# Kernel optimization log

Hardware: AMD Instinct MI355X
Metric: run time of the kernel (lower is better)

## Reference

```python
import jax, jax.numpy as jnp
import numpy as np

K = 1024
H = 128

def setup_inputs() -> dict:
    key = jax.random.key(0)
    ks = jax.random.split(key, 11)
    s = lambda fan_in: 1.0 / np.sqrt(fan_in)
    # coord_mlp: Linear(H, H//2) -> GELU -> Linear(H//2, 2)
    cW1 = jax.random.uniform(ks[0], (H, H // 2), minval=-s(H), maxval=s(H))
    cb1 = jax.random.uniform(ks[1], (H // 2,), minval=-s(H), maxval=s(H))
    cW2 = jax.random.uniform(ks[2], (H // 2, 2), minval=-s(H // 2), maxval=s(H // 2))
    cb2 = jax.random.uniform(ks[3], (2,), minval=-s(H // 2), maxval=s(H // 2))
    # edge_mlp: Linear(2H, H) -> GELU -> Linear(H, H//2) -> GELU -> Linear(H//2, 1)
    eW1 = jax.random.uniform(ks[4], (2 * H, H), minval=-s(2 * H), maxval=s(2 * H))
    eb1 = jax.random.uniform(ks[5], (H,), minval=-s(2 * H), maxval=s(2 * H))
    eW2 = jax.random.uniform(ks[6], (H, H // 2), minval=-s(H), maxval=s(H))
    eb2 = jax.random.uniform(ks[7], (H // 2,), minval=-s(H), maxval=s(H))
    eW3 = jax.random.uniform(ks[8], (H // 2, 1), minval=-s(H // 2), maxval=s(H // 2))
    eb3 = jax.random.uniform(ks[9], (1,), minval=-s(H // 2), maxval=s(H // 2))
    z_s = jax.random.normal(ks[10], (K, H), dtype=jnp.float32)
    return {"z_s": z_s, "cW1": cW1, "cb1": cb1, "cW2": cW2, "cb2": cb2,
            "eW1": eW1, "eb1": eb1, "eW2": eW2, "eb2": eb2, "eW3": eW3, "eb3": eb3}

def reference(z_s, cW1, cb1, cW2, cb2, eW1, eb1, eW2, eb2, eW3, eb3):
    gelu = lambda x: jax.nn.gelu(x, approximate=False)  # torch default GELU is exact erf form
    # coords: [k, 2]
    coords_pred = gelu(z_s @ cW1 + cb1) @ cW2 + cb2
    # edge first layer: cat([zi, zj]) @ eW1 == zi @ eW1[:H] + zj @ eW1[H:]
    # (same math as the broadcast-concat, without materializing [k, k, 2H])
    pi = z_s @ eW1[:H]   # [k, H]
    pj = z_s @ eW1[H:]   # [k, H]
    h1 = gelu(pi[:, None, :] + pj[None, :, :] + eb1)   # [k, k, H]
    h2 = gelu(h1 @ eW2 + eb2)                          # [k, k, H//2]
    adj_logits = (h2 @ eW3 + eb3)[..., 0]              # [k, k]
    adj_logits = (adj_logits + adj_logits.T) / 2.0
    return (coords_pred, adj_logits)
```

## Files before the change

### kernel.cpp

```cpp
#include <hip/hip_runtime.h>
#include <hip/hip_fp16.h>


#define KN 1024
#define HN 128

typedef float  floatx4 __attribute__((ext_vector_type(4)));
typedef _Float16 half8v __attribute__((ext_vector_type(8)));
typedef _Float16 half2v __attribute__((ext_vector_type(2)));

__device__ __forceinline__ float gelu_f(float x) {
    float x2 = x * x;
    float t  = fmaf(x2, -0.1029434f, -2.3022087f);
    float e  = __builtin_amdgcn_exp2f(x * t);
    return x * __builtin_amdgcn_rcpf(e + 1.0f);
}

__device__ __forceinline__ unsigned int gelu2u(unsigned int xu) {
    __half2 x  = __builtin_bit_cast(__half2, xu);
    __half2 x2 = __hmul2(x, x);
    __half2 t  = __hfma2(x2, __float2half2_rn(-0.1029434f),
                             __float2half2_rn(-2.3022087f));
    __half2 e  = h2exp2(__hmul2(x, t));
    __half2 r  = h2rcp(__hadd2(e, __float2half2_rn(1.0f)));
    return __builtin_bit_cast(unsigned int, __hmul2(x, r));
}

__device__ __forceinline__ unsigned int cvt2u(float a, float b) {
    return __builtin_bit_cast(unsigned int, __builtin_amdgcn_cvt_pkrtz(a, b));
}

__global__ __launch_bounds__(256) void prep_kernel(
    const float* __restrict__ z,   const float* __restrict__ cW1,
    const float* __restrict__ cb1, const float* __restrict__ cW2,
    const float* __restrict__ cb2, const float* __restrict__ eW1,
    const float* __restrict__ eb1, const float* __restrict__ eW2,
    const float* __restrict__ eW3,
    _Float16* __restrict__ pi_h,   _Float16* __restrict__ pj_h,
    _Float16* __restrict__ w2T,    _Float16* __restrict__ w3h,
    float* __restrict__ coords ) {
    __shared__ float z8[8][128];
    __shared__ float c1s[8][64];
    const int tid = threadIdx.x;
    const int r0  = blockIdx.x * 8;

    if (blockIdx.x < 32) {
        int e = blockIdx.x * 256 + tid;
        int d = e >> 7, k = e & 127;
        int R = ((d >> 5) & 1) * 32 + ((d >> 2) & 1) * 16 +
                ((d >> 3) & 3) * 4  + (d & 3);
        w2T[R * 128 + k] = (_Float16)eW2[k * 64 + d];
    }
    if (blockIdx.x == 32 && tid < 64) w3h[tid] = (_Float16)eW3[tid];

#pragma unroll
    for (int s = 0; s < 4; ++s) {
        int e = tid + 256 * s;
        z8[e >> 7][e & 127] = z[r0 * HN + e];
    }
    __syncthreads();

    const int col = tid & 127, which = tid >> 7;
    const float* w = eW1 + which * HN * HN + col;
    float acc8[8] = {0.f, 0.f, 0.f, 0.f, 0.f, 0.f, 0.f, 0.f};
    for (int k = 0; k < HN; ++k) {
        float wv = w[k * HN];
#pragma unroll
        for (int r = 0; r < 8; ++r) acc8[r] = fmaf(z8[r][k], wv, acc8[r]);
    }
    if (which == 0) {
        float b = eb1[col];
#pragma unroll
        for (int r = 0; r < 8; ++r)
            pi_h[(r0 + r) * HN + col] = (_Float16)(acc8[r] + b);
    } else {
#pragma unroll
        for (int r = 0; r < 8; ++r)
            pj_h[(r0 + r) * HN + col] = (_Float16)acc8[r];
    }

#pragma unroll
    for (int s = 0; s < 2; ++s) {
        int task = tid + 256 * s;
        int row = task >> 6, mid = task & 63;
        float a = cb1[mid];
        for (int k = 0; k < HN; ++k) a = fmaf(z8[row][k], cW1[k * 64 + mid], a);
        c1s[row][mid] = gelu_f(a);
    }
    __syncthreads();
    if (tid < 16) {
        int row = tid >> 1, o = tid & 1;
        float a = cb2[o];
#pragma unroll 8
        for (int m = 0; m < 64; ++m) a = fmaf(c1s[row][m], cW2[m * 2 + o], a);
        coords[(r0 + row) * 2 + o] = a;
    }
}

__global__ __launch_bounds__(512, 7) void edge_kernel(
    const _Float16* __restrict__ pi_h, const _Float16* __restrict__ pj_h,
    const _Float16* __restrict__ w2T,  const _Float16* __restrict__ w3h,
    const float* __restrict__ eb2,     const float* __restrict__ eb3,
    float* __restrict__ out_adj) {
    __shared__ __align__(16) unsigned int pi_s[32 * 64];
    __shared__ __align__(16) unsigned int pj_s[16 * 64];
    __shared__ __align__(16) unsigned int w2_s[64 * 64];
    const int i0 = blockIdx.y * 32, j0 = blockIdx.x * 16;
    const int tid = threadIdx.x;

    const unsigned int* piu = (const unsigned int*)pi_h;
    const unsigned int* pju = (const unsigned int*)pj_h;
    const unsigned int* w2u = (const unsigned int*)w2T;

#pragma unroll
    for (int s = 0; s < 4; ++s) {
        int e = tid + 512 * s;
        int r = e >> 6;
        pi_s[e ^ ((r & 7) << 2)] = piu[(i0 + r) * 64 + (e & 63)];
    }
#pragma unroll
    for (int s = 0; s < 2; ++s) {
        int e = tid + 512 * s;
        int r = e >> 6;
        pj_s[e ^ ((r & 7) << 2)] = pju[(j0 + r) * 64 + (e & 63)];
    }
#pragma unroll
    for (int s = 0; s < 8; ++s) {
        int e = tid + 512 * s;
        int r = e >> 6;
        w2_s[e ^ ((r & 7) << 2)] = w2u[e];
    }

    const int lane = tid & 63;
    const int wave = tid >> 6;
    const int lrow = lane & 15;
    const int lhi  = lane >> 4;
    const int lhi4 = lhi << 2;
    const int lhi8 = lhi << 3;
    const int swzJ = (lrow & 7) << 2;

    const unsigned int* pjrow  = &pj_s[lrow << 6];
    const unsigned int* w2base = &w2_s[lrow << 6];

    const half8v w3f0 = *reinterpret_cast<const half8v*>(&w3h[lhi8]);
    const half8v w3f1 = *reinterpret_cast<const half8v*>(&w3h[32 + lhi8]);
    const float4 e0 = *reinterpret_cast<const float4*>(&eb2[lhi8]);
    const float4 e1 = *reinterpret_cast<const float4*>(&eb2[lhi8 + 4]);
    const float4 e2 = *reinterpret_cast<const float4*>(&eb2[32 + lhi8]);
    const float4 e3 = *reinterpret_cast<const float4*>(&eb2[36 + lhi8]);
    const float b3 = eb3[0];
    __syncthreads();

#pragma unroll
    for (int t = 0; t < 4; ++t) {
        const int iL = (wave << 2) + t;
        const unsigned int* pirow = &pi_s[iL << 6];
        const int swzI = (iL & 7) << 2;

        floatx4 acc[4];
        acc[0] = (floatx4){e0.x, e0.y, e0.z, e0.w};
        acc[1] = (floatx4){e1.x, e1.y, e1.z, e1.w};
        acc[2] = (floatx4){e2.x, e2.y, e2.z, e2.w};
        acc[3] = (floatx4){e3.x, e3.y, e3.z, e3.w};

#pragma unroll
        for (int q = 0; q < 4; ++q) {
            const int ko = (q << 4) + lhi4;
            half8v a = *reinterpret_cast<const half8v*>(&pirow[ko ^ swzI]);
            half8v b = *reinterpret_cast<const half8v*>(&pjrow[ko ^ swzJ]);
            uint4 su = __builtin_bit_cast(uint4, a + b);
            uint4 gu;
            gu.x = gelu2u(su.x);
            gu.y = gelu2u(su.y);
            gu.z = gelu2u(su.z);
            gu.w = gelu2u(su.w);
            half8v af = __builtin_bit_cast(half8v, gu);
            const int kw = ko ^ swzJ;
#pragma unroll
            for (int c = 0; c < 4; ++c) {
                half8v bf = *reinterpret_cast<const half8v*>(
                    &w2base[(c << 10) + kw]);
                acc[c] = __builtin_amdgcn_mfma_f32_16x16x32_f16(
                    bf, af, acc[c], 0, 0, 0);
            }
        }

        uint4 u0, u1;
        u0.x = gelu2u(cvt2u(acc[0][0], acc[0][1]));
        u0.y = gelu2u(cvt2u(acc[0][2], acc[0][3]));
        u0.z = gelu2u(cvt2u(acc[1][0], acc[1][1]));
        u0.w = gelu2u(cvt2u(acc[1][2], acc[1][3]));
        u1.x = gelu2u(cvt2u(acc[2][0], acc[2][1]));
        u1.y = gelu2u(cvt2u(acc[2][2], acc[2][3]));
        u1.z = gelu2u(cvt2u(acc[3][0], acc[3][1]));
        u1.w = gelu2u(cvt2u(acc[3][2], acc[3][3]));
        half8v h20 = __builtin_bit_cast(half8v, u0);
        half8v h21 = __builtin_bit_cast(half8v, u1);

        floatx4 d = (floatx4){b3, b3, b3, b3};
        d = __builtin_amdgcn_mfma_f32_16x16x32_f16(w3f0, h20, d, 0, 0, 0);
        d = __builtin_amdgcn_mfma_f32_16x16x32_f16(w3f1, h21, d, 0, 0, 0);
        if (lhi == 0)
            out_adj[(size_t)(i0 + iL) * KN + j0 + lrow] = d[0];
    }
}

__global__ __launch_bounds__(256) void sym_kernel(float* __restrict__ adj) {
    int idx = blockIdx.x * 256 + threadIdx.x;
    int i = idx >> 10, j = idx & 1023;
    if (j < i) return;
    float a = adj[i * KN + j];
    float b = adj[j * KN + i];
    float m = 0.5f * (a + b);
    adj[i * KN + j] = m;
    adj[j * KN + i] = m;
}

extern "C" void kernel_launch(void* const* d_in, const int* in_sizes, int n_in,
                              void* d_out, int out_size, void* d_ws, size_t ws_size,
                              hipStream_t stream) {
    const float* z   = (const float*)d_in[0];
    const float* cW1 = (const float*)d_in[1];
    const float* cb1 = (const float*)d_in[2];
    const float* cW2 = (const float*)d_in[3];
    const float* cb2 = (const float*)d_in[4];
    const float* eW1 = (const float*)d_in[5];
    const float* eb1 = (const float*)d_in[6];
    const float* eW2 = (const float*)d_in[7];
    const float* eb2 = (const float*)d_in[8];
    const float* eW3 = (const float*)d_in[9];
    const float* eb3 = (const float*)d_in[10];

    float* out = (float*)d_out;
    _Float16* pi_h = (_Float16*)d_ws;
    _Float16* pj_h = pi_h + KN * HN;
    _Float16* w2T  = pj_h + KN * HN;
    _Float16* w3h  = w2T + 64 * HN;

    prep_kernel<<<128, 256, 0, stream>>>(z, cW1, cb1, cW2, cb2, eW1, eb1, eW2,
                                         eW3, pi_h, pj_h, w2T, w3h, out);

    dim3 gridB(64, 32);
    edge_kernel<<<gridB, 512, 0, stream>>>(pi_h, pj_h, w2T, w3h, eb2, eb3,
                                           out + 2048);

    sym_kernel<<<4096, 256, 0, stream>>>(out + 2048);
}
```

Measured before the change: 79.48 us.

## Enlarge edge tiles to 64x32 and reuse W2 fragments across two j-subtiles

Each edge-kernel block now covers 64 i-rows by 32 j-columns, and each wave handles 8 i-rows. Per k-step, every W2 fragment read from LDS feeds two MFMAs, one per 16-column j half. The pj fragments are hoisted into registers once per wave. This cuts LDS traffic for W2 and pj per output and amortises tile loads over more work, at the cost of higher register pressure (occupancy hint lowered to 4) and fewer blocks (512 instead of 2048). The prep kernel is also reshaped to 512-thread blocks covering 16 rows each.

New measurement: 80.96 us. About the same (+1.9%).

```diff
diff --git a/kernel.cpp b/kernel.cpp
--- a/kernel.cpp
+++ b/kernel.cpp
@@ -7,7 +7,6 @@
 
 typedef float  floatx4 __attribute__((ext_vector_type(4)));
 typedef _Float16 half8v __attribute__((ext_vector_type(8)));
-typedef _Float16 half2v __attribute__((ext_vector_type(2)));
 
 __device__ __forceinline__ float gelu_f(float x) {
     float x2 = x * x;
@@ -30,7 +29,26 @@
     return __builtin_bit_cast(unsigned int, __builtin_amdgcn_cvt_pkrtz(a, b));
 }
 
-__global__ __launch_bounds__(256) void prep_kernel(
+__device__ __forceinline__ float dotw3(const floatx4* acc, half8v w3f0,
+                                       half8v w3f1, float b3) {
+    uint4 u0, u1;
+    u0.x = gelu2u(cvt2u(acc[0][0], acc[0][1]));
+    u0.y = gelu2u(cvt2u(acc[0][2], acc[0][3]));
+    u0.z = gelu2u(cvt2u(acc[1][0], acc[1][1]));
+    u0.w = gelu2u(cvt2u(acc[1][2], acc[1][3]));
+    u1.x = gelu2u(cvt2u(acc[2][0], acc[2][1]));
+    u1.y = gelu2u(cvt2u(acc[2][2], acc[2][3]));
+    u1.z = gelu2u(cvt2u(acc[3][0], acc[3][1]));
+    u1.w = gelu2u(cvt2u(acc[3][2], acc[3][3]));
+    half8v h20 = __builtin_bit_cast(half8v, u0);
+    half8v h21 = __builtin_bit_cast(half8v, u1);
+    floatx4 d = (floatx4){b3, b3, b3, b3};
+    d = __builtin_amdgcn_mfma_f32_16x16x32_f16(w3f0, h20, d, 0, 0, 0);
+    d = __builtin_amdgcn_mfma_f32_16x16x32_f16(w3f1, h21, d, 0, 0, 0);
+    return d[0];
+}
+
+__global__ __launch_bounds__(512) void prep_kernel(
     const float* __restrict__ z,   const float* __restrict__ cW1,
     const float* __restrict__ cb1, const float* __restrict__ cW2,
     const float* __restrict__ cb2, const float* __restrict__ eW1,
@@ -39,56 +57,58 @@
     _Float16* __restrict__ pi_h,   _Float16* __restrict__ pj_h,
     _Float16* __restrict__ w2T,    _Float16* __restrict__ w3h,
     float* __restrict__ coords ) {
-    __shared__ float z8[8][128];
-    __shared__ float c1s[8][64];
+    __shared__ float z16[16][128];
+    __shared__ float c1s[16][64];
     const int tid = threadIdx.x;
-    const int r0  = blockIdx.x * 8;
-
-    if (blockIdx.x < 32) {
-        int e = blockIdx.x * 256 + tid;
+    const int r0  = blockIdx.x * 16;
+
+    if (blockIdx.x < 16) {
+        int e = blockIdx.x * 512 + tid;
         int d = e >> 7, k = e & 127;
         int R = ((d >> 5) & 1) * 32 + ((d >> 2) & 1) * 16 +
                 ((d >> 3) & 3) * 4  + (d & 3);
         w2T[R * 128 + k] = (_Float16)eW2[k * 64 + d];
     }
-    if (blockIdx.x == 32 && tid < 64) w3h[tid] = (_Float16)eW3[tid];
+    if (blockIdx.x == 16 && tid < 64) w3h[tid] = (_Float16)eW3[tid];
 
 #pragma unroll
     for (int s = 0; s < 4; ++s) {
-        int e = tid + 256 * s;
-        z8[e >> 7][e & 127] = z[r0 * HN + e];
+        int e = tid + 512 * s;
+        z16[e >> 7][e & 127] = z[r0 * HN + e];
     }
     __syncthreads();
 
     const int col = tid & 127, which = tid >> 7;
-    const float* w = eW1 + which * HN * HN + col;
+    const int sel = which & 1, half = which >> 1;
+    const float* w = eW1 + sel * HN * HN + col;
     float acc8[8] = {0.f, 0.f, 0.f, 0.f, 0.f, 0.f, 0.f, 0.f};
     for (int k = 0; k < HN; ++k) {
         float wv = w[k * HN];
 #pragma unroll
-        for (int r = 0; r < 8; ++r) acc8[r] = fmaf(z8[r][k], wv, acc8[r]);
-    }
-    if (which == 0) {
+        for (int r = 0; r < 8; ++r)
+            acc8[r] = fmaf(z16[half * 8 + r][k], wv, acc8[r]);
+    }
+    if (sel == 0) {
         float b = eb1[col];
 #pragma unroll
         for (int r = 0; r < 8; ++r)
-            pi_h[(r0 + r) * HN + col] = (_Float16)(acc8[r] + b);
+            pi_h[(r0 + half * 8 + r) * HN + col] = (_Float16)(acc8[r] + b);
     } else {
 #pragma unroll
         for (int r = 0; r < 8; ++r)
-            pj_h[(r0 + r) * HN + col] = (_Float16)acc8[r];
+            pj_h[(r0 + half * 8 + r) * HN + col] = (_Float16)acc8[r];
     }
 
 #pragma unroll
     for (int s = 0; s < 2; ++s) {
-        int task = tid + 256 * s;
+        int task = tid + 512 * s;
         int row = task >> 6, mid = task & 63;
         float a = cb1[mid];
-        for (int k = 0; k < HN; ++k) a = fmaf(z8[row][k], cW1[k * 64 + mid], a);
+        for (int k = 0; k < HN; ++k) a = fmaf(z16[row][k], cW1[k * 64 + mid], a);
         c1s[row][mid] = gelu_f(a);
     }
     __syncthreads();
-    if (tid < 16) {
+    if (tid < 32) {
         int row = tid >> 1, o = tid & 1;
         float a = cb2[o];
 #pragma unroll 8
@@ -97,15 +117,15 @@
     }
 }
 
-__global__ __launch_bounds__(512, 7) void edge_kernel(
+__global__ __launch_bounds__(512, 4) void edge_kernel(
     const _Float16* __restrict__ pi_h, const _Float16* __restrict__ pj_h,
     const _Float16* __restrict__ w2T,  const _Float16* __restrict__ w3h,
     const float* __restrict__ eb2,     const float* __restrict__ eb3,
     float* __restrict__ out_adj) {
-    __shared__ __align__(16) unsigned int pi_s[32 * 64];
-    __shared__ __align__(16) unsigned int pj_s[16 * 64];
+    __shared__ __align__(16) unsigned int pi_s[64 * 64];
+    __shared__ __align__(16) unsigned int pj_s[32 * 64];
     __shared__ __align__(16) unsigned int w2_s[64 * 64];
-    const int i0 = blockIdx.y * 32, j0 = blockIdx.x * 16;
+    const int i0 = blockIdx.y * 64, j0 = blockIdx.x * 32;
     const int tid = threadIdx.x;
 
     const unsigned int* piu = (const unsigned int*)pi_h;
@@ -113,13 +133,13 @@
     const unsigned int* w2u = (const unsigned int*)w2T;
 
 #pragma unroll
-    for (int s = 0; s < 4; ++s) {
+    for (int s = 0; s < 8; ++s) {
         int e = tid + 512 * s;
         int r = e >> 6;
         pi_s[e ^ ((r & 7) << 2)] = piu[(i0 + r) * 64 + (e & 63)];
     }
 #pragma unroll
-    for (int s = 0; s < 2; ++s) {
+    for (int s = 0; s < 4; ++s) {
         int e = tid + 512 * s;
         int r = e >> 6;
         pj_s[e ^ ((r & 7) << 2)] = pju[(j0 + r) * 64 + (e & 63)];
@@ -138,9 +158,6 @@
     const int lhi4 = lhi << 2;
     const int lhi8 = lhi << 3;
     const int swzJ = (lrow & 7) << 2;
-
-    const unsigned int* pjrow  = &pj_s[lrow << 6];
-    const unsigned int* w2base = &w2_s[lrow << 6];
 
     const half8v w3f0 = *reinterpret_cast<const half8v*>(&w3h[lhi8]);
     const half8v w3f1 = *reinterpret_cast<const half8v*>(&w3h[32 + lhi8]);
@@ -151,57 +168,67 @@
     const float b3 = eb3[0];
     __syncthreads();
 
-#pragma unroll
-    for (int t = 0; t < 4; ++t) {
-        const int iL = (wave << 2) + t;
+    const unsigned int* pjA = &pj_s[lrow << 6];
+    const unsigned int* pjB = &pj_s[(16 + lrow) << 6];
+    half8v bA[4], bB[4];
+#pragma unroll
+    for (int q = 0; q < 4; ++q) {
+        const int ko = ((q << 4) | lhi4) ^ swzJ;
+        bA[q] = *reinterpret_cast<const half8v*>(&pjA[ko]);
+        bB[q] = *reinterpret_cast<const half8v*>(&pjB[ko]);
+    }
+    const unsigned int* w2base = &w2_s[lrow << 6];
+
+#pragma unroll
+    for (int t = 0; t < 8; ++t) {
+        const int iL = (wave << 3) + t;
         const unsigned int* pirow = &pi_s[iL << 6];
-        const int swzI = (iL & 7) << 2;
-
-        floatx4 acc[4];
-        acc[0] = (floatx4){e0.x, e0.y, e0.z, e0.w};
-        acc[1] = (floatx4){e1.x, e1.y, e1.z, e1.w};
-        acc[2] = (floatx4){e2.x, e2.y, e2.z, e2.w};
-        acc[3] = (floatx4){e3.x, e3.y, e3.z, e3.w};
+        const int swzI = t << 2;
+
+        floatx4 accA[4], accB[4];
+        accA[0] = (floatx4){e0.x, e0.y, e0.z, e0.w};
+        accA[1] = (floatx4){e1.x, e1.y, e1.z, e1.w};
+        accA[2] = (floatx4){e2.x, e2.y, e2.z, e2.w};
+        accA[3] = (floatx4){e3.x, e3.y, e3.z, e3.w};
+#pragma unroll
+        for (int c = 0; c < 4; ++c) accB[c] = accA[c];
 
 #pragma unroll
         for (int q = 0; q < 4; ++q) {
-            const int ko = (q << 4) + lhi4;
+            const int ko = (q << 4) | lhi4;
             half8v a = *reinterpret_cast<const half8v*>(&pirow[ko ^ swzI]);
-            half8v b = *reinterpret_cast<const half8v*>(&pjrow[ko ^ swzJ]);
-            uint4 su = __builtin_bit_cast(uint4, a + b);
-            uint4 gu;
-            gu.x = gelu2u(su.x);
-            gu.y = gelu2u(su.y);
-            gu.z = gelu2u(su.z);
-            gu.w = gelu2u(su.w);
-            half8v af = __builtin_bit_cast(half8v, gu);
+
+            uint4 sA = __builtin_bit_cast(uint4, a + bA[q]);
+            uint4 gA;
+            gA.x = gelu2u(sA.x); gA.y = gelu2u(sA.y);
+            gA.z = gelu2u(sA.z); gA.w = gelu2u(sA.w);
+            half8v afA = __builtin_bit_cast(half8v, gA);
+
+            uint4 sB = __builtin_bit_cast(uint4, a + bB[q]);
+            uint4 gB;
+            gB.x = gelu2u(sB.x); gB.y = gelu2u(sB.y);
+            gB.z = gelu2u(sB.z); gB.w = gelu2u(sB.w);
+            half8v afB = __builtin_bit_cast(half8v, gB);
+
             const int kw = ko ^ swzJ;
 #pragma unroll
             for (int c = 0; c < 4; ++c) {
                 half8v bf = *reinterpret_cast<const half8v*>(
                     &w2base[(c << 10) + kw]);
-                acc[c] = __builtin_amdgcn_mfma_f32_16x16x32_f16(
-                    bf, af, acc[c], 0, 0, 0);
+                accA[c] = __builtin_amdgcn_mfma_f32_16x16x32_f16(
+                    bf, afA, accA[c], 0, 0, 0);
+                accB[c] = __builtin_amdgcn_mfma_f32_16x16x32_f16(
+                    bf, afB, accB[c], 0, 0, 0);
             }
         }
 
-        uint4 u0, u1;
-        u0.x = gelu2u(cvt2u(acc[0][0], acc[0][1]));
-        u0.y = gelu2u(cvt2u(acc[0][2], acc[0][3]));
-        u0.z = gelu2u(cvt2u(acc[1][0], acc[1][1]));
-        u0.w = gelu2u(cvt2u(acc[1][2], acc[1][3]));
-        u1.x = gelu2u(cvt2u(acc[2][0], acc[2][1]));
-        u1.y = gelu2u(cvt2u(acc[2][2], acc[2][3]));
-        u1.z = gelu2u(cvt2u(acc[3][0], acc[3][1]));
-        u1.w = gelu2u(cvt2u(acc[3][2], acc[3][3]));
-        half8v h20 = __builtin_bit_cast(half8v, u0);
-        half8v h21 = __builtin_bit_cast(half8v, u1);
-
-        floatx4 d = (floatx4){b3, b3, b3, b3};
-        d = __builtin_amdgcn_mfma_f32_16x16x32_f16(w3f0, h20, d, 0, 0, 0);
-        d = __builtin_amdgcn_mfma_f32_16x16x32_f16(w3f1, h21, d, 0, 0, 0);
-        if (lhi == 0)
-            out_adj[(size_t)(i0 + iL) * KN + j0 + lrow] = d[0];
+        const float dA = dotw3(accA, w3f0, w3f1, b3);
+        const float dB = dotw3(accB, w3f0, w3f1, b3);
+        if (lhi == 0) {
+            float* row = &out_adj[(size_t)(i0 + iL) * KN + j0];
+            row[lrow]      = dA;
+            row[16 + lrow] = dB;
+        }
     }
 }
 
@@ -237,10 +264,10 @@
     _Float16* w2T  = pj_h + KN * HN;
     _Float16* w3h  = w2T + 64 * HN;
 
-    prep_kernel<<<128, 256, 0, stream>>>(z, cW1, cb1, cW2, cb2, eW1, eb1, eW2,
-                                         eW3, pi_h, pj_h, w2T, w3h, out);
-
-    dim3 gridB(64, 32);
+    prep_kernel<<<64, 512, 0, stream>>>(z, cW1, cb1, cW2, cb2, eW1, eb1, eW2,
+                                        eW3, pi_h, pj_h, w2T, w3h, out);
+
+    dim3 gridB(32, 16);
     edge_kernel<<<gridB, 512, 0, stream>>>(pi_h, pj_h, w2T, w3h, eb2, eb3,
                                            out + 2048);
 
```
